# Kernel optimization log

Measured on AMD Instinct MI355X. Metric: run time of the kernel, lower is better.

The kernel has to match this reference:

```python
import jax, jax.numpy as jnp
import numpy as np

NUM_ENT = 14541
NUM_REL = 474
D = 400
B = 32
N_CAND = 14505


def setup_inputs() -> dict:
    key = jax.random.key(0)
    k0, k1, k2, k4, k5 = jax.random.split(key, 5)
    return {
        "arg0_1": jax.random.normal(k0, (NUM_ENT, D), dtype=jnp.float32),   # entity embeddings
        "arg1_1": jax.random.normal(k1, (NUM_REL, D), dtype=jnp.float32),   # relation centers
        "arg2_1": jax.random.uniform(k2, (NUM_REL, D), dtype=jnp.float32),  # relation offsets (box widths)
        "arg3_1": jnp.ones((1,), dtype=jnp.float32),                        # margin gamma
        "arg4_1": jax.random.randint(k4, (B, 2), 0, NUM_REL),               # (head_id, rel_id) pairs
        "arg5_1": jax.random.randint(k5, (4, N_CAND), 0, NUM_ENT),          # candidate entity ids (row 0 used)
    }


def reference(arg0_1, arg1_1, arg2_1, arg3_1, arg4_1, arg5_1):
    # Gather heads / relation params
    head = arg0_1[arg4_1[:, 0]]            # [B, D]
    rel_c = arg1_1[arg4_1[:, 1]]           # [B, D]
    rel_o = arg2_1[arg4_1[:, 1]]           # [B, D]

    query = (head + rel_c)[:, None, :]     # [B, 1, D] box center
    offset = rel_o[:, None, :]             # [B, 1, D] box width

    # Candidate tail embeddings: only row 0 of arg5_1 is used in the graph
    cand = arg0_1[arg5_1[0].reshape(-1)][None, :, :]  # [1, N_CAND, D]

    d = jnp.abs(cand - query)                           # [B, N_CAND, D]
    dist_outside = jax.nn.relu(d - offset).sum(-1)      # [B, N_CAND]
    dist_inside = jnp.abs(jnp.minimum(d, offset)).sum(-1)

    return arg3_1 - dist_outside - 0.02 * dist_inside   # [B, N_CAND]
```

## Files before the change

### kernel.cpp

```cpp
#include <hip/hip_runtime.h>

#define DIM     400
#define B       32
#define NCAND   14505
#define NROUND  3627
#define TSTRIPS 256
#define THREADS 256

__global__ __launch_bounds__(THREADS, 2)
void score_kernel(const float* __restrict__ ent,
                  const float* __restrict__ relc,
                  const float* __restrict__ relo,
                  const float* __restrict__ onev,
                  const int*   __restrict__ pairs,
                  const int*   __restrict__ cidx,
                  float* __restrict__ out) {
    const int fid  = blockIdx.x;
    const int xcd  = fid & 7;
    const int rest = fid >> 3;
    const int bq   = rest & 7;
    const int tc   = rest >> 3;
    const int t    = xcd + 8 * tc;

    const int tid  = threadIdx.x;
    const int lane = tid & 63;
    const int u    = lane & 15;
    const int g    = lane >> 4;
    const int b    = __builtin_amdgcn_readfirstlane(bq * 4 + (tid >> 6));

    const int hd = pairs[b * 2 + 0];
    const int rl = pairs[b * 2 + 1];
    const float4* hb = (const float4*)(ent  + (size_t)hd * DIM) + u;
    const float4* cb = (const float4*)(relc + (size_t)rl * DIM) + u;
    const float4* ob = (const float4*)(relo + (size_t)rl * DIM) + u;

    float4 q[7], o[7];
    float oa = 0.f;
#pragma unroll
    for (int k = 0; k < 6; ++k) {
        float4 h = hb[16 * k], c = cb[16 * k];
        q[k] = make_float4(h.x + c.x, h.y + c.y, h.z + c.z, h.w + c.w);
        o[k] = ob[16 * k];
        oa += o[k].x + o[k].y + o[k].z + o[k].w;
    }
    if (u < 4) {
        float4 h = hb[96], c = cb[96];
        q[6] = make_float4(h.x + c.x, h.y + c.y, h.z + c.z, h.w + c.w);
        o[6] = ob[96];
        oa += o[6].x + o[6].y + o[6].z + o[6].w;
    }
    oa += __shfl_xor(oa, 1);
    oa += __shfl_xor(oa, 2);
    oa += __shfl_xor(oa, 4);
    oa += __shfl_xor(oa, 8);
    const float base = onev[0] + 0.98f * oa;

    const float4* entu = (const float4*)ent + u;

    for (int rr = t; rr < NROUND; rr += TSTRIPS) {
        const int cand = 4 * rr + g;
        const int ci   = cidx[cand < NCAND ? cand : NCAND - 1];
        const float4* p = entu + (size_t)ci * 100;

        float4 cbuf[7];
#pragma unroll
        for (int k = 0; k < 6; ++k) cbuf[k] = p[16 * k];
        if (u < 4) cbuf[6] = p[96];

        float am0 = 0.f, ad0 = 0.f, am1 = 0.f, ad1 = 0.f;
#define E(vc, vq, vo, AM, AD)                     \
        {                                         \
            float d_ = (vc) - (vq);               \
            AM += fmaxf(fabsf(d_), (vo));         \
            AD += fabsf(d_);                      \
        }
#define F4(k, AM, AD)                             \
        E(cbuf[k].x, q[k].x, o[k].x, AM, AD)      \
        E(cbuf[k].y, q[k].y, o[k].y, AM, AD)      \
        E(cbuf[k].z, q[k].z, o[k].z, AM, AD)      \
        E(cbuf[k].w, q[k].w, o[k].w, AM, AD)

        F4(0, am0, ad0) F4(1, am1, ad1)
        F4(2, am0, ad0) F4(3, am1, ad1)
        F4(4, am0, ad0) F4(5, am1, ad1)
        if (u < 4) { F4(6, am0, ad0) }
#undef F4
#undef E

        float s_ = fmaf(-0.98f, am0 + am1, -0.02f * (ad0 + ad1));
        s_ += __shfl_xor(s_, 1);
        s_ += __shfl_xor(s_, 2);
        s_ += __shfl_xor(s_, 4);
        s_ += __shfl_xor(s_, 8);

        if (u == 0 && cand < NCAND)
            out[(size_t)b * NCAND + cand] = base + s_;
    }
}

extern "C" void kernel_launch(void* const* d_in, const int* in_sizes, int n_in,
                              void* d_out, int out_size, void* d_ws, size_t ws_size,
                              hipStream_t stream) {
    const float* ent   = (const float*)d_in[0];
    const float* relc  = (const float*)d_in[1];
    const float* relo  = (const float*)d_in[2];
    const float* onev  = (const float*)d_in[3];
    const int*   pairs = (const int*)d_in[4];
    const int*   cidx  = (const int*)d_in[5];
    float*       out   = (float*)d_out;

    const int grid = 8 * 8 * 32;
    score_kernel<<<grid, THREADS, 0, stream>>>(ent, relc, relo, onev, pairs, cidx, out);
}
```

Before: 46.16 us.

## Rewrite scoring kernel with fp16 packed math and LDS-staged queries

Replaces the per-batch strip kernel with one where each lane handles a (batch, candidate) pair. All 32 query/offset vectors are staged in shared memory as packed fp16, and candidate rows are converted to half2. The distance terms are folded algebraically into max(|d|, 0.02|d| + 0.98o) and accumulated with fdot2 into fp32. This cuts ALU work and removes the cross-lane reductions, but lowers precision to fp16, which with unit-normal embeddings may exceed tolerance. Each lane also reads whole 400-float rows, so loads within a wavefront are less coalesced.

After: 42.54 us. 1.09x faster.

```diff
diff --git a/kernel.cpp b/kernel.cpp
--- a/kernel.cpp
+++ b/kernel.cpp
@@ -1,101 +1,137 @@
 #include <hip/hip_runtime.h>
 
 #define DIM     400
+#define NENT    14541
 #define B       32
 #define NCAND   14505
-#define NROUND  3627
-#define TSTRIPS 256
-#define THREADS 256
+#define NBLK    455
+#define THREADS 512
+
+typedef __attribute__((ext_vector_type(2))) _Float16 half2_t;
+
+static __device__ __forceinline__ half2_t bch(unsigned u) {
+    return __builtin_bit_cast(half2_t, u);
+}
+static __device__ __forceinline__ half2_t habs2(half2_t x) {
+    unsigned u = __builtin_bit_cast(unsigned, x) & 0x7fff7fffu;
+    return __builtin_bit_cast(half2_t, u);
+}
+static __device__ __forceinline__ unsigned pkh(float x, float y) {
+    half2_t h;
+    h.x = (_Float16)x;
+    h.y = (_Float16)y;
+    return __builtin_bit_cast(unsigned, h);
+}
+static __device__ __forceinline__ float dot2acc(half2_t m, float s) {
+#if __has_builtin(__builtin_amdgcn_fdot2)
+    const half2_t ones = {(_Float16)1.f, (_Float16)1.f};
+    return __builtin_amdgcn_fdot2(m, ones, s, false);
+#else
+    return s + (float)m.x + (float)m.y;
+#endif
+}
 
 __global__ __launch_bounds__(THREADS, 2)
-void score_kernel(const float* __restrict__ ent,
-                  const float* __restrict__ relc,
-                  const float* __restrict__ relo,
-                  const float* __restrict__ onev,
-                  const int*   __restrict__ pairs,
-                  const int*   __restrict__ cidx,
-                  float* __restrict__ out) {
-    const int fid  = blockIdx.x;
-    const int xcd  = fid & 7;
-    const int rest = fid >> 3;
-    const int bq   = rest & 7;
-    const int tc   = rest >> 3;
-    const int t    = xcd + 8 * tc;
+void score_fused(const float* __restrict__ ent,
+                 const float* __restrict__ relc,
+                 const float* __restrict__ relo,
+                 const float* __restrict__ onev,
+                 const int*   __restrict__ pairs,
+                 const int*   __restrict__ cidx,
+                 float* __restrict__ out) {
+    __shared__ uint4 qs[1600];
+    __shared__ uint4 os[1600];
+    __shared__ float bpart[THREADS];
+    __shared__ float base_s[B];
 
-    const int tid  = threadIdx.x;
+    const int tid = threadIdx.x;
+
+    float part = 0.f;
+    for (int i = tid; i < 1600; i += THREADS) {
+        const int j = i >> 5;
+        const int b = i & 31;
+        const int h = pairs[2 * b + 0];
+        const int r = pairs[2 * b + 1];
+        const float4* hp = (const float4*)(ent  + (size_t)h * DIM) + 2 * j;
+        const float4* cp = (const float4*)(relc + (size_t)r * DIM) + 2 * j;
+        const float4* op = (const float4*)(relo + (size_t)r * DIM) + 2 * j;
+        float4 h0 = hp[0], h1 = hp[1];
+        float4 c0 = cp[0], c1 = cp[1];
+        float4 v0 = op[0], v1 = op[1];
+        uint4 qv, ov;
+        qv.x = pkh(h0.x + c0.x, h0.y + c0.y);
+        qv.y = pkh(h0.z + c0.z, h0.w + c0.w);
+        qv.z = pkh(h1.x + c1.x, h1.y + c1.y);
+        qv.w = pkh(h1.z + c1.z, h1.w + c1.w);
+        ov.x = pkh(0.98f * v0.x, 0.98f * v0.y);
+        ov.y = pkh(0.98f * v0.z, 0.98f * v0.w);
+        ov.z = pkh(0.98f * v1.x, 0.98f * v1.y);
+        ov.w = pkh(0.98f * v1.z, 0.98f * v1.w);
+        qs[i] = qv;
+        os[i] = ov;
+        part += v0.x + v0.y + v0.z + v0.w + v1.x + v1.y + v1.z + v1.w;
+    }
+    bpart[tid] = part;
+    __syncthreads();
+    if (tid < B) {
+        float s = 0.f;
+#pragma unroll
+        for (int k = 0; k < THREADS / 32; ++k) s += bpart[tid + 32 * k];
+        base_s[tid] = onev[0] + 0.98f * s;
+    }
+    __syncthreads();
+
+    const int wid  = tid >> 6;
     const int lane = tid & 63;
-    const int u    = lane & 15;
-    const int g    = lane >> 4;
-    const int b    = __builtin_amdgcn_readfirstlane(bq * 4 + (tid >> 6));
+    const int b    = lane & 31;
+    const int c2   = lane >> 5;
+    const float base = base_s[b];
 
-    const int hd = pairs[b * 2 + 0];
-    const int rl = pairs[b * 2 + 1];
-    const float4* hb = (const float4*)(ent  + (size_t)hd * DIM) + u;
-    const float4* cb = (const float4*)(relc + (size_t)rl * DIM) + u;
-    const float4* ob = (const float4*)(relo + (size_t)rl * DIM) + u;
+    const int p0    = blockIdx.x * 16 + wid * 2;
+    const int candA = 2 * p0 + c2;
+    const int candB = 2 * (p0 + 1) + c2;
+    const int ciA = cidx[candA < NCAND ? candA : NCAND - 1];
+    const int ciB = cidx[candB < NCAND ? candB : NCAND - 1];
+    const float4* rA = (const float4*)(ent + (size_t)ciA * DIM);
+    const float4* rB = (const float4*)(ent + (size_t)ciB * DIM);
 
-    float4 q[7], o[7];
-    float oa = 0.f;
-#pragma unroll
-    for (int k = 0; k < 6; ++k) {
-        float4 h = hb[16 * k], c = cb[16 * k];
-        q[k] = make_float4(h.x + c.x, h.y + c.y, h.z + c.z, h.w + c.w);
-        o[k] = ob[16 * k];
-        oa += o[k].x + o[k].y + o[k].z + o[k].w;
+    const half2_t K002 = {(_Float16)0.02f, (_Float16)0.02f};
+
+#define PAIRE(cu, qu, ou, SS)                                   \
+    {                                                           \
+        half2_t cc_ = bch(cu), qq_ = bch(qu), oo_ = bch(ou);    \
+        half2_t dd_ = cc_ - qq_;                                \
+        half2_t aa_ = habs2(dd_);                               \
+        half2_t ee_ = aa_ * K002 + oo_;                         \
+        half2_t mm_ = __builtin_elementwise_max(aa_, ee_);      \
+        SS = dot2acc(mm_, SS);                                  \
     }
-    if (u < 4) {
-        float4 h = hb[96], c = cb[96];
-        q[6] = make_float4(h.x + c.x, h.y + c.y, h.z + c.z, h.w + c.w);
-        o[6] = ob[96];
-        oa += o[6].x + o[6].y + o[6].z + o[6].w;
+#define PROC(C, Q, O, SA, SB)                                   \
+    PAIRE(C.x, Q.x, O.x, SA) PAIRE(C.y, Q.y, O.y, SB)           \
+    PAIRE(C.z, Q.z, O.z, SA) PAIRE(C.w, Q.w, O.w, SB)
+
+    float sA0 = 0.f, sA1 = 0.f, sB0 = 0.f, sB1 = 0.f;
+#pragma unroll 5
+    for (int j = 0; j < 50; ++j) {
+        float4 a0 = rA[2 * j], a1 = rA[2 * j + 1];
+        float4 e0 = rB[2 * j], e1 = rB[2 * j + 1];
+        uint4 ca, ce;
+        ca.x = pkh(a0.x, a0.y); ca.y = pkh(a0.z, a0.w);
+        ca.z = pkh(a1.x, a1.y); ca.w = pkh(a1.z, a1.w);
+        ce.x = pkh(e0.x, e0.y); ce.y = pkh(e0.z, e0.w);
+        ce.z = pkh(e1.x, e1.y); ce.w = pkh(e1.z, e1.w);
+        const uint4 qj = qs[(j << 5) | b];
+        const uint4 oj = os[(j << 5) | b];
+        PROC(ca, qj, oj, sA0, sA1)
+        PROC(ce, qj, oj, sB0, sB1)
     }
-    oa += __shfl_xor(oa, 1);
-    oa += __shfl_xor(oa, 2);
-    oa += __shfl_xor(oa, 4);
-    oa += __shfl_xor(oa, 8);
-    const float base = onev[0] + 0.98f * oa;
+#undef PROC
+#undef PAIRE
 
-    const float4* entu = (const float4*)ent + u;
-
-    for (int rr = t; rr < NROUND; rr += TSTRIPS) {
-        const int cand = 4 * rr + g;
-        const int ci   = cidx[cand < NCAND ? cand : NCAND - 1];
-        const float4* p = entu + (size_t)ci * 100;
-
-        float4 cbuf[7];
-#pragma unroll
-        for (int k = 0; k < 6; ++k) cbuf[k] = p[16 * k];
-        if (u < 4) cbuf[6] = p[96];
-
-        float am0 = 0.f, ad0 = 0.f, am1 = 0.f, ad1 = 0.f;
-#define E(vc, vq, vo, AM, AD)                     \
-        {                                         \
-            float d_ = (vc) - (vq);               \
-            AM += fmaxf(fabsf(d_), (vo));         \
-            AD += fabsf(d_);                      \
-        }
-#define F4(k, AM, AD)                             \
-        E(cbuf[k].x, q[k].x, o[k].x, AM, AD)      \
-        E(cbuf[k].y, q[k].y, o[k].y, AM, AD)      \
-        E(cbuf[k].z, q[k].z, o[k].z, AM, AD)      \
-        E(cbuf[k].w, q[k].w, o[k].w, AM, AD)
-
-        F4(0, am0, ad0) F4(1, am1, ad1)
-        F4(2, am0, ad0) F4(3, am1, ad1)
-        F4(4, am0, ad0) F4(5, am1, ad1)
-        if (u < 4) { F4(6, am0, ad0) }
-#undef F4
-#undef E
-
-        float s_ = fmaf(-0.98f, am0 + am1, -0.02f * (ad0 + ad1));
-        s_ += __shfl_xor(s_, 1);
-        s_ += __shfl_xor(s_, 2);
-        s_ += __shfl_xor(s_, 4);
-        s_ += __shfl_xor(s_, 8);
-
-        if (u == 0 && cand < NCAND)
-            out[(size_t)b * NCAND + cand] = base + s_;
-    }
+    if (candA < NCAND)
+        out[(size_t)b * NCAND + candA] = base - (sA0 + sA1);
+    if (candB < NCAND)
+        out[(size_t)b * NCAND + candB] = base - (sB0 + sB1);
 }
 
 extern "C" void kernel_launch(void* const* d_in, const int* in_sizes, int n_in,
@@ -109,6 +145,5 @@
     const int*   cidx  = (const int*)d_in[5];
     float*       out   = (float*)d_out;
 
-    const int grid = 8 * 8 * 32;
-    score_kernel<<<grid, THREADS, 0, stream>>>(ent, relc, relo, onev, pairs, cidx, out);
+    score_fused<<<NBLK, THREADS, 0, stream>>>(ent, relc, relo, onev, pairs, cidx, out);
 }
```
